# Performance work log

Measured on AMD Instinct MI355X. Metric: run time of the kernel, lower is better.

## Reference

```python
import jax, jax.numpy as jnp
import numpy as np

PAD = 1  # deform_conv2d called with stride=1, padding=1, dilation=1 in forward


def _bilinear_gather(x, py, px):
    """Bilinear sample x [B,C,H,W] at float coords py,px [B,K,Ho,Wo].
    Out-of-bounds corners contribute zero (torchvision deform_conv2d semantics).
    Returns [B,C,K,Ho,Wo]."""
    B, C, H, W = x.shape
    y0 = jnp.floor(py)
    x0 = jnp.floor(px)
    y1, x1 = y0 + 1.0, x0 + 1.0
    wy1 = py - y0
    wy0 = 1.0 - wy1
    wx1 = px - x0
    wx0 = 1.0 - wx1
    x_flat = x.reshape(B, C, H * W)

    def corner(yi, xi, w):
        m = ((yi >= 0) & (yi < H) & (xi >= 0) & (xi < W)).astype(x.dtype)
        yc = jnp.clip(yi, 0, H - 1).astype(jnp.int32)
        xc = jnp.clip(xi, 0, W - 1).astype(jnp.int32)
        lin = (yc * W + xc).reshape(B, -1)  # [B, K*Ho*Wo]
        vals = jax.vmap(lambda xf, idx: jnp.take(xf, idx, axis=1))(x_flat, lin)
        vals = vals.reshape(B, C, *yi.shape[1:])  # [B,C,K,Ho,Wo]
        return vals * (w * m)[:, None]

    return (corner(y0, x0, wy0 * wx0) + corner(y0, x1, wy0 * wx1)
            + corner(y1, x0, wy1 * wx0) + corner(y1, x1, wy1 * wx1))


def reference(x, w_off, b_off, weight):
    B, C, H, W = x.shape
    O, Ci, kh, kw = weight.shape
    K = kh * kw
    # offset conv: Conv2d(C -> 2*k*k, kernel 3, stride 1, pad 1, groups=1)
    offset = jax.lax.conv_general_dilated(
        x, w_off, window_strides=(1, 1), padding=[(PAD, PAD), (PAD, PAD)],
        dimension_numbers=('NCHW', 'OIHW', 'NCHW')) + b_off[None, :, None, None]
    off = offset.reshape(B, K, 2, H, W)  # channel layout: (tap, [dy, dx])

    ky = jnp.repeat(jnp.arange(kh, dtype=x.dtype), kw)  # [K] kernel row index
    kx = jnp.tile(jnp.arange(kw, dtype=x.dtype), kh)    # [K] kernel col index
    ys = jnp.arange(H, dtype=x.dtype)[None, None, :, None]  # [1,1,H,1]
    xs = jnp.arange(W, dtype=x.dtype)[None, None, None, :]  # [1,1,1,W]
    py = ys + (ky - PAD)[None, :, None, None] + off[:, :, 0]  # [B,K,H,W]
    px = xs + (kx - PAD)[None, :, None, None] + off[:, :, 1]

    sampled = _bilinear_gather(x, py, px)  # [B,C,K,H,W]
    out = jnp.einsum('bckhw,ock->bohw', sampled, weight.reshape(O, Ci, K))
    return out


def setup_inputs() -> dict:
    key = jax.random.key(0)
    k1, k2, k3 = jax.random.split(key, 3)
    x = jax.random.normal(k1, (4, 64, 128, 128), dtype=jnp.float32)
    # small offset-conv weights -> modest learned offsets (realistic DCN behavior)
    w_off = jax.random.normal(k2, (18, 64, 3, 3), dtype=jnp.float32) * 0.01
    b_off = jnp.zeros((18,), dtype=jnp.float32)
    weight = jax.random.normal(k3, (64, 64, 3, 3), dtype=jnp.float32)
    return {'x': x, 'w_off': w_off, 'b_off': b_off, 'weight': weight}
```

## Files before the change

kernel.cpp:

```cpp
#include <hip/hip_runtime.h>
#include <math.h>

typedef _Float16 f16;
typedef _Float16 f16x8 __attribute__((ext_vector_type(8)));
typedef float f32x4 __attribute__((ext_vector_type(4)));

namespace {
constexpr int Bn = 4;
constexpr int Cn = 64;
constexpr int On = 64;
constexpr int Hn = 128;
constexpr int Wn = 128;
constexpr int Kn = 9;
constexpr int HWn = Hn * Wn;
constexpr int NPIX = Bn * HWn;
constexpr int SR = 72;
}

__global__ __launch_bounds__(256) void transpose_prep(
    const float* __restrict__ x, const float* __restrict__ w_off,
    const float* __restrict__ weight, f16* __restrict__ xt,
    f16* __restrict__ wofb, f16* __restrict__ wtb) {
  const int l = threadIdx.x & 63;
  const int cw = threadIdx.x >> 6;
  const int pixbase = blockIdx.x * 64;
  const int b = pixbase >> 14;
  const int hw = (pixbase & (HWn - 1)) + l;

  f16x8 v0, v1;
#pragma unroll
  for (int i = 0; i < 8; ++i) {
    v0[i] = (f16)x[((size_t)(b * Cn + cw * 16 + i)) * HWn + hw];
    v1[i] = (f16)x[((size_t)(b * Cn + cw * 16 + 8 + i)) * HWn + hw];
  }
  f16* dst = xt + ((size_t)(b * HWn + hw)) * 64 + cw * 16;
  *(f16x8*)dst = v0;
  *(f16x8*)(dst + 8) = v1;

  if (blockIdx.x < 144) {
    int t = blockIdx.x * 256 + threadIdx.x;
    {
      int c = t & 63, o = (t >> 6) & 63, k = t >> 12;
      wtb[t] = (f16)weight[((o << 6) + c) * 9 + k];
    }
    if (t < Kn * 32 * Cn) {
      int c = t & 63, o = (t >> 6) & 31, k = t >> 11;
      float v = (o < 18) ? w_off[((o << 6) + c) * 9 + k] : 0.f;
      wofb[t] = (f16)v;
    }
  }
}

__global__ __launch_bounds__(128, 4) void dcn_fused(
    const f16* __restrict__ xt, const f16* __restrict__ wofb,
    const f16* __restrict__ wtb, const float* __restrict__ b_off,
    float* __restrict__ out) {
  __shared__ __align__(16) f16 Sb[3][32 * SR];
  __shared__ float off_lds[32][20];

  const int t = threadIdx.x;
  const int px_s = t >> 2, cq = t & 3;
  const int pixbase = blockIdx.x * 32;
  const int b = pixbase >> 14;
  const int y = (pixbase & (HWn - 1)) >> 7;
  const int xx0 = pixbase & (Wn - 1);
  const int xx = xx0 + px_s;
  const f16* xb = xt + ((size_t)b * HWn) * 64;

  const int lane = t & 63, wv = t >> 6;
  const int l15 = lane & 15, q = lane >> 4;

  {
    f32x4 accA[2];
#pragma unroll
    for (int pt = 0; pt < 2; ++pt) accA[pt] = (f32x4){0.f, 0.f, 0.f, 0.f};

    for (int g = 0; g < 3; ++g) {
      if (g) __syncthreads();

      f16x8 wfA[3][2];
#pragma unroll
      for (int j = 0; j < 3; ++j)
#pragma unroll
        for (int s = 0; s < 2; ++s)
          wfA[j][s] = *(const f16x8*)(wofb +
              (((size_t)((3 * g + j) * 32 + wv * 16 + l15)) << 6) +
              s * 32 + q * 8);

#pragma unroll
      for (int j = 0; j < 3; ++j) {
        const int k = 3 * g + j;
        const int dy = k / 3 - 1, dx = k % 3 - 1;
        const int ys = y + dy, xs = xx + dx;
        f16* sdst = &Sb[j][px_s * SR + cq * 16];
        if (ys >= 0 && ys < Hn && xs >= 0 && xs < Wn) {
          const f16* src = xb + (size_t)(ys * Wn + xs) * 64 + cq * 16;
          *(f16x8*)sdst = *(const f16x8*)src;
          *(f16x8*)(sdst + 8) = *(const f16x8*)(src + 8);
        } else {
          f16x8 z = {};
          *(f16x8*)sdst = z;
          *(f16x8*)(sdst + 8) = z;
        }
      }
      __syncthreads();

#pragma unroll
      for (int j = 0; j < 3; ++j)
#pragma unroll
        for (int s = 0; s < 2; ++s)
#pragma unroll
          for (int pt = 0; pt < 2; ++pt) {
            f16x8 bf = *(const f16x8*)
                &Sb[j][(pt * 16 + l15) * SR + s * 32 + q * 8];
            accA[pt] = __builtin_amdgcn_mfma_f32_16x16x32_f16(wfA[j][s], bf,
                                                              accA[pt],
                                                              0, 0, 0);
          }
    }

#pragma unroll
    for (int pt = 0; pt < 2; ++pt)
#pragma unroll
      for (int r = 0; r < 4; ++r) {
        int o = wv * 16 + q * 4 + r;
        if (o < 18) {
          int pxl = pt * 16 + l15;
          off_lds[pxl][o] = accA[pt][r] + b_off[o];
        }
      }
    __syncthreads();
  }

  float2 off9[9];
#pragma unroll
  for (int k = 0; k < Kn; ++k)
    off9[k] = *(const float2*)&off_lds[px_s][2 * k];

  f32x4 acc[2][2];
#pragma unroll
  for (int ot = 0; ot < 2; ++ot)
#pragma unroll
    for (int pt = 0; pt < 2; ++pt) acc[ot][pt] = (f32x4){0.f, 0.f, 0.f, 0.f};

  for (int g = 0; g < 3; ++g) {
    if (g) __syncthreads();

    f16x8 wf[3][2][2];
#pragma unroll
    for (int j = 0; j < 3; ++j)
#pragma unroll
      for (int ot = 0; ot < 2; ++ot)
#pragma unroll
        for (int s = 0; s < 2; ++s)
          wf[j][ot][s] = *(const f16x8*)(wtb +
              (((size_t)((3 * g + j) * 64 + wv * 32 + ot * 16 + l15)) << 6) +
              s * 32 + q * 8);

#pragma unroll
    for (int j = 0; j < 3; ++j) {
      const int k = 3 * g + j;
      const int dy = k / 3 - 1, dx = k % 3 - 1;
      float py = (float)(y + dy) + off9[k].x;
      float pxf = (float)(xx + dx) + off9[k].y;
      float y0f = floorf(py), x0f = floorf(pxf);
      int y0 = (int)y0f, x0 = (int)x0f;
      int y1 = y0 + 1, x1 = x0 + 1;
      float wy1 = py - y0f, wx1 = pxf - x0f;
      float wy0 = 1.f - wy1, wx0 = 1.f - wx1;
      float my0 = (y0 >= 0 && y0 < Hn) ? 1.f : 0.f;
      float my1 = (y1 >= 0 && y1 < Hn) ? 1.f : 0.f;
      float mx0 = (x0 >= 0 && x0 < Wn) ? 1.f : 0.f;
      float mx1 = (x1 >= 0 && x1 < Wn) ? 1.f : 0.f;
      f16 h00 = (f16)(wy0 * wx0 * my0 * mx0);
      f16 h01 = (f16)(wy0 * wx1 * my0 * mx1);
      f16 h10 = (f16)(wy1 * wx0 * my1 * mx0);
      f16 h11 = (f16)(wy1 * wx1 * my1 * mx1);
      int cy0 = min(max(y0, 0), Hn - 1), cy1 = min(max(y1, 0), Hn - 1);
      int cx0 = min(max(x0, 0), Wn - 1), cx1 = min(max(x1, 0), Wn - 1);
      const f16* r00 = xb + (size_t)(cy0 * Wn + cx0) * 64 + cq * 16;
      const f16* r01 = xb + (size_t)(cy0 * Wn + cx1) * 64 + cq * 16;
      const f16* r10 = xb + (size_t)(cy1 * Wn + cx0) * 64 + cq * 16;
      const f16* r11 = xb + (size_t)(cy1 * Wn + cx1) * 64 + cq * 16;
      f16* sdst = &Sb[j][px_s * SR + cq * 16];
#pragma unroll
      for (int h = 0; h < 2; ++h) {
        f16x8 a = *(const f16x8*)(r00 + h * 8);
        f16x8 b2 = *(const f16x8*)(r01 + h * 8);
        f16x8 c = *(const f16x8*)(r10 + h * 8);
        f16x8 d = *(const f16x8*)(r11 + h * 8);
        f16x8 v = a * h00 + b2 * h01 + c * h10 + d * h11;
        *(f16x8*)(sdst + h * 8) = v;
      }
    }
    __syncthreads();

#pragma unroll
    for (int j = 0; j < 3; ++j)
#pragma unroll
      for (int s = 0; s < 2; ++s)
#pragma unroll
        for (int pt = 0; pt < 2; ++pt) {
          f16x8 bf =
              *(const f16x8*)&Sb[j][(pt * 16 + l15) * SR + s * 32 + q * 8];
#pragma unroll
          for (int ot = 0; ot < 2; ++ot)
            acc[ot][pt] = __builtin_amdgcn_mfma_f32_16x16x32_f16(
                wf[j][ot][s], bf, acc[ot][pt], 0, 0, 0);
        }
  }

  float* ob = out + (size_t)b * On * HWn + (y * Wn + xx0);
#pragma unroll
  for (int ot = 0; ot < 2; ++ot)
#pragma unroll
    for (int pt = 0; pt < 2; ++pt)
#pragma unroll
      for (int r = 0; r < 4; ++r) {
        int o = wv * 32 + ot * 16 + q * 4 + r;
        ob[(size_t)o * HWn + pt * 16 + l15] = acc[ot][pt][r];
      }
}

extern "C" void kernel_launch(void* const* d_in, const int* in_sizes, int n_in,
                              void* d_out, int out_size, void* d_ws, size_t ws_size,
                              hipStream_t stream) {
  const float* x = (const float*)d_in[0];
  const float* w_off = (const float*)d_in[1];
  const float* b_off = (const float*)d_in[2];
  const float* weight = (const float*)d_in[3];
  float* out = (float*)d_out;

  f16* xt = (f16*)d_ws;
  f16* wtb = xt + (size_t)NPIX * Cn;
  f16* wofb = wtb + Kn * On * Cn;

  transpose_prep<<<dim3(NPIX / 64), dim3(256), 0, stream>>>(x, w_off, weight,
                                                            xt, wofb, wtb);
  dcn_fused<<<dim3(NPIX / 32), dim3(128), 0, stream>>>(xt, wofb, wtb, b_off,
                                                       out);
}
```

Baseline: 114.3 us.

## Restructure fused DCN kernel to single-wave blocks without barriers

```diff
diff --git a/kernel.cpp b/kernel.cpp
--- a/kernel.cpp
+++ b/kernel.cpp
@@ -51,175 +51,147 @@
   }
 }
 
-__global__ __launch_bounds__(128, 4) void dcn_fused(
+__global__ __launch_bounds__(64, 3) void dcn_wave(
     const f16* __restrict__ xt, const f16* __restrict__ wofb,
     const f16* __restrict__ wtb, const float* __restrict__ b_off,
     float* __restrict__ out) {
-  __shared__ __align__(16) f16 Sb[3][32 * SR];
-  __shared__ float off_lds[32][20];
-
-  const int t = threadIdx.x;
-  const int px_s = t >> 2, cq = t & 3;
-  const int pixbase = blockIdx.x * 32;
+  __shared__ __align__(16) f16 Sb[2][16 * SR];
+  __shared__ float off_lds[16][20];
+
+  const int l = threadIdx.x;
+  const int px_s = l >> 2, cq = l & 3;
+  const int pixbase = blockIdx.x * 16;
   const int b = pixbase >> 14;
   const int y = (pixbase & (HWn - 1)) >> 7;
   const int xx0 = pixbase & (Wn - 1);
   const int xx = xx0 + px_s;
   const f16* xb = xt + ((size_t)b * HWn) * 64;
-
-  const int lane = t & 63, wv = t >> 6;
-  const int l15 = lane & 15, q = lane >> 4;
-
-  {
-    f32x4 accA[2];
-#pragma unroll
-    for (int pt = 0; pt < 2; ++pt) accA[pt] = (f32x4){0.f, 0.f, 0.f, 0.f};
-
-    for (int g = 0; g < 3; ++g) {
-      if (g) __syncthreads();
-
-      f16x8 wfA[3][2];
-#pragma unroll
-      for (int j = 0; j < 3; ++j)
-#pragma unroll
-        for (int s = 0; s < 2; ++s)
-          wfA[j][s] = *(const f16x8*)(wofb +
-              (((size_t)((3 * g + j) * 32 + wv * 16 + l15)) << 6) +
-              s * 32 + q * 8);
-
-#pragma unroll
-      for (int j = 0; j < 3; ++j) {
-        const int k = 3 * g + j;
-        const int dy = k / 3 - 1, dx = k % 3 - 1;
-        const int ys = y + dy, xs = xx + dx;
-        f16* sdst = &Sb[j][px_s * SR + cq * 16];
-        if (ys >= 0 && ys < Hn && xs >= 0 && xs < Wn) {
-          const f16* src = xb + (size_t)(ys * Wn + xs) * 64 + cq * 16;
-          *(f16x8*)sdst = *(const f16x8*)src;
-          *(f16x8*)(sdst + 8) = *(const f16x8*)(src + 8);
-        } else {
-          f16x8 z = {};
-          *(f16x8*)sdst = z;
-          *(f16x8*)(sdst + 8) = z;
-        }
-      }
-      __syncthreads();
-
-#pragma unroll
-      for (int j = 0; j < 3; ++j)
-#pragma unroll
-        for (int s = 0; s < 2; ++s)
-#pragma unroll
-          for (int pt = 0; pt < 2; ++pt) {
-            f16x8 bf = *(const f16x8*)
-                &Sb[j][(pt * 16 + l15) * SR + s * 32 + q * 8];
-            accA[pt] = __builtin_amdgcn_mfma_f32_16x16x32_f16(wfA[j][s], bf,
-                                                              accA[pt],
-                                                              0, 0, 0);
-          }
-    }
-
-#pragma unroll
-    for (int pt = 0; pt < 2; ++pt)
-#pragma unroll
-      for (int r = 0; r < 4; ++r) {
-        int o = wv * 16 + q * 4 + r;
-        if (o < 18) {
-          int pxl = pt * 16 + l15;
-          off_lds[pxl][o] = accA[pt][r] + b_off[o];
-        }
-      }
-    __syncthreads();
-  }
+  const int l15 = l & 15, q = l >> 4;
+
+  f32x4 accA[2];
+#pragma unroll
+  for (int m = 0; m < 2; ++m) accA[m] = (f32x4){0.f, 0.f, 0.f, 0.f};
+
+#pragma unroll
+  for (int k = 0; k < Kn; ++k) {
+    const int dy = k / 3 - 1, dx = k % 3 - 1;
+    const int ys = y + dy, xs = xx + dx;
+    f16x8 s0 = {}, s1 = {};
+    if (ys >= 0 && ys < Hn && xs >= 0 && xs < Wn) {
+      const f16* src = xb + (size_t)(ys * Wn + xs) * 64 + cq * 16;
+      s0 = *(const f16x8*)src;
+      s1 = *(const f16x8*)(src + 8);
+    }
+    f16x8 wfA[2][2];
+#pragma unroll
+    for (int m = 0; m < 2; ++m)
+#pragma unroll
+      for (int s = 0; s < 2; ++s)
+        wfA[m][s] = *(const f16x8*)(wofb +
+            (((size_t)(k * 32 + m * 16 + l15)) << 6) + s * 32 + q * 8);
+
+    f16* sd = &Sb[k & 1][px_s * SR + cq * 16];
+    *(f16x8*)sd = s0;
+    *(f16x8*)(sd + 8) = s1;
+
+    f16x8 bf[2];
+#pragma unroll
+    for (int s = 0; s < 2; ++s)
+      bf[s] = *(const f16x8*)&Sb[k & 1][l15 * SR + s * 32 + q * 8];
+#pragma unroll
+    for (int s = 0; s < 2; ++s)
+#pragma unroll
+      for (int m = 0; m < 2; ++m)
+        accA[m] = __builtin_amdgcn_mfma_f32_16x16x32_f16(wfA[m][s], bf[s],
+                                                         accA[m], 0, 0, 0);
+  }
+
+#pragma unroll
+  for (int m = 0; m < 2; ++m)
+#pragma unroll
+    for (int r = 0; r < 4; ++r) {
+      int o = m * 16 + q * 4 + r;
+      if (o < 18) off_lds[l15][o] = accA[m][r] + b_off[o];
+    }
 
   float2 off9[9];
 #pragma unroll
   for (int k = 0; k < Kn; ++k)
     off9[k] = *(const float2*)&off_lds[px_s][2 * k];
 
-  f32x4 acc[2][2];
-#pragma unroll
-  for (int ot = 0; ot < 2; ++ot)
-#pragma unroll
-    for (int pt = 0; pt < 2; ++pt) acc[ot][pt] = (f32x4){0.f, 0.f, 0.f, 0.f};
-
-  for (int g = 0; g < 3; ++g) {
-    if (g) __syncthreads();
-
-    f16x8 wf[3][2][2];
-#pragma unroll
-    for (int j = 0; j < 3; ++j)
-#pragma unroll
-      for (int ot = 0; ot < 2; ++ot)
-#pragma unroll
-        for (int s = 0; s < 2; ++s)
-          wf[j][ot][s] = *(const f16x8*)(wtb +
-              (((size_t)((3 * g + j) * 64 + wv * 32 + ot * 16 + l15)) << 6) +
-              s * 32 + q * 8);
-
-#pragma unroll
-    for (int j = 0; j < 3; ++j) {
-      const int k = 3 * g + j;
-      const int dy = k / 3 - 1, dx = k % 3 - 1;
-      float py = (float)(y + dy) + off9[k].x;
-      float pxf = (float)(xx + dx) + off9[k].y;
-      float y0f = floorf(py), x0f = floorf(pxf);
-      int y0 = (int)y0f, x0 = (int)x0f;
-      int y1 = y0 + 1, x1 = x0 + 1;
-      float wy1 = py - y0f, wx1 = pxf - x0f;
-      float wy0 = 1.f - wy1, wx0 = 1.f - wx1;
-      float my0 = (y0 >= 0 && y0 < Hn) ? 1.f : 0.f;
-      float my1 = (y1 >= 0 && y1 < Hn) ? 1.f : 0.f;
-      float mx0 = (x0 >= 0 && x0 < Wn) ? 1.f : 0.f;
-      float mx1 = (x1 >= 0 && x1 < Wn) ? 1.f : 0.f;
-      f16 h00 = (f16)(wy0 * wx0 * my0 * mx0);
-      f16 h01 = (f16)(wy0 * wx1 * my0 * mx1);
-      f16 h10 = (f16)(wy1 * wx0 * my1 * mx0);
-      f16 h11 = (f16)(wy1 * wx1 * my1 * mx1);
-      int cy0 = min(max(y0, 0), Hn - 1), cy1 = min(max(y1, 0), Hn - 1);
-      int cx0 = min(max(x0, 0), Wn - 1), cx1 = min(max(x1, 0), Wn - 1);
-      const f16* r00 = xb + (size_t)(cy0 * Wn + cx0) * 64 + cq * 16;
-      const f16* r01 = xb + (size_t)(cy0 * Wn + cx1) * 64 + cq * 16;
-      const f16* r10 = xb + (size_t)(cy1 * Wn + cx0) * 64 + cq * 16;
-      const f16* r11 = xb + (size_t)(cy1 * Wn + cx1) * 64 + cq * 16;
-      f16* sdst = &Sb[j][px_s * SR + cq * 16];
-#pragma unroll
-      for (int h = 0; h < 2; ++h) {
-        f16x8 a = *(const f16x8*)(r00 + h * 8);
-        f16x8 b2 = *(const f16x8*)(r01 + h * 8);
-        f16x8 c = *(const f16x8*)(r10 + h * 8);
-        f16x8 d = *(const f16x8*)(r11 + h * 8);
-        f16x8 v = a * h00 + b2 * h01 + c * h10 + d * h11;
-        *(f16x8*)(sdst + h * 8) = v;
-      }
-    }
-    __syncthreads();
-
-#pragma unroll
-    for (int j = 0; j < 3; ++j)
+  f32x4 acc[4];
+#pragma unroll
+  for (int m = 0; m < 4; ++m) acc[m] = (f32x4){0.f, 0.f, 0.f, 0.f};
+
+#pragma unroll
+  for (int k = 0; k < Kn; ++k) {
+    const int dy = k / 3 - 1, dx = k % 3 - 1;
+    float py = (float)(y + dy) + off9[k].x;
+    float pxf = (float)(xx + dx) + off9[k].y;
+    float y0f = floorf(py), x0f = floorf(pxf);
+    int y0 = (int)y0f, x0 = (int)x0f;
+    int y1 = y0 + 1, x1 = x0 + 1;
+    float wy1 = py - y0f, wx1 = pxf - x0f;
+    float wy0 = 1.f - wy1, wx0 = 1.f - wx1;
+    float my0 = (y0 >= 0 && y0 < Hn) ? 1.f : 0.f;
+    float my1 = (y1 >= 0 && y1 < Hn) ? 1.f : 0.f;
+    float mx0 = (x0 >= 0 && x0 < Wn) ? 1.f : 0.f;
+    float mx1 = (x1 >= 0 && x1 < Wn) ? 1.f : 0.f;
+    f16 h00 = (f16)(wy0 * wx0 * my0 * mx0);
+    f16 h01 = (f16)(wy0 * wx1 * my0 * mx1);
+    f16 h10 = (f16)(wy1 * wx0 * my1 * mx0);
+    f16 h11 = (f16)(wy1 * wx1 * my1 * mx1);
+    int cy0 = min(max(y0, 0), Hn - 1), cy1 = min(max(y1, 0), Hn - 1);
+    int cx0 = min(max(x0, 0), Wn - 1), cx1 = min(max(x1, 0), Wn - 1);
+
+    const f16* r00 = xb + (size_t)(cy0 * Wn + cx0) * 64 + cq * 16;
+    const f16* r01 = xb + (size_t)(cy0 * Wn + cx1) * 64 + cq * 16;
+    const f16* r10 = xb + (size_t)(cy1 * Wn + cx0) * 64 + cq * 16;
+    const f16* r11 = xb + (size_t)(cy1 * Wn + cx1) * 64 + cq * 16;
+    f16x8 cr[4][2];
+#pragma unroll
+    for (int h = 0; h < 2; ++h) {
+      cr[0][h] = *(const f16x8*)(r00 + h * 8);
+      cr[1][h] = *(const f16x8*)(r01 + h * 8);
+      cr[2][h] = *(const f16x8*)(r10 + h * 8);
+      cr[3][h] = *(const f16x8*)(r11 + h * 8);
+    }
+    f16x8 wf[4][2];
+#pragma unroll
+    for (int m = 0; m < 4; ++m)
 #pragma unroll
       for (int s = 0; s < 2; ++s)
-#pragma unroll
-        for (int pt = 0; pt < 2; ++pt) {
-          f16x8 bf =
-              *(const f16x8*)&Sb[j][(pt * 16 + l15) * SR + s * 32 + q * 8];
-#pragma unroll
-          for (int ot = 0; ot < 2; ++ot)
-            acc[ot][pt] = __builtin_amdgcn_mfma_f32_16x16x32_f16(
-                wf[j][ot][s], bf, acc[ot][pt], 0, 0, 0);
-        }
-  }
-
-  float* ob = out + (size_t)b * On * HWn + (y * Wn + xx0);
-#pragma unroll
-  for (int ot = 0; ot < 2; ++ot)
-#pragma unroll
-    for (int pt = 0; pt < 2; ++pt)
-#pragma unroll
-      for (int r = 0; r < 4; ++r) {
-        int o = wv * 32 + ot * 16 + q * 4 + r;
-        ob[(size_t)o * HWn + pt * 16 + l15] = acc[ot][pt][r];
-      }
+        wf[m][s] = *(const f16x8*)(wtb +
+            (((size_t)(k * 64 + m * 16 + l15)) << 6) + s * 32 + q * 8);
+
+    f16* sd = &Sb[k & 1][px_s * SR + cq * 16];
+#pragma unroll
+    for (int h = 0; h < 2; ++h) {
+      f16x8 v = cr[0][h] * h00 + cr[1][h] * h01 +
+                cr[2][h] * h10 + cr[3][h] * h11;
+      *(f16x8*)(sd + h * 8) = v;
+    }
+
+    f16x8 bf[2];
+#pragma unroll
+    for (int s = 0; s < 2; ++s)
+      bf[s] = *(const f16x8*)&Sb[k & 1][l15 * SR + s * 32 + q * 8];
+#pragma unroll
+    for (int s = 0; s < 2; ++s)
+#pragma unroll
+      for (int m = 0; m < 4; ++m)
+        acc[m] = __builtin_amdgcn_mfma_f32_16x16x32_f16(wf[m][s], bf[s],
+                                                        acc[m], 0, 0, 0);
+  }
+
+  float* ob = out + (size_t)b * On * HWn + y * Wn + xx0;
+#pragma unroll
+  for (int m = 0; m < 4; ++m)
+#pragma unroll
+    for (int r = 0; r < 4; ++r) {
+      int o = m * 16 + q * 4 + r;
+      ob[(size_t)o * HWn + l15] = acc[m][r];
+    }
 }
 
 extern "C" void kernel_launch(void* const* d_in, const int* in_sizes, int n_in,
@@ -237,6 +209,6 @@
 
   transpose_prep<<<dim3(NPIX / 64), dim3(256), 0, stream>>>(x, w_off, weight,
                                                             xt, wofb, wtb);
-  dcn_fused<<<dim3(NPIX / 32), dim3(128), 0, stream>>>(xt, wofb, wtb, b_off,
-                                                       out);
-}
+  dcn_wave<<<dim3(NPIX / 16), dim3(64), 0, stream>>>(xt, wofb, wtb, b_off,
+                                                     out);
+}
```

Measured after the change: 137.8 us. +20.6%, slower.
